# Optimization experiments

Measured on AMD Instinct MI355X. Metric: run time of the kernel, lower is better.

The kernel has to match this reference:

```python
import jax, jax.numpy as jnp
import numpy as np

LN_EPS = 1e-5


def lstm_cell(x, h, c, Wih, Whh, b):
    # PyTorch gate order: i, f, g, o
    gates = x @ Wih.T + h @ Whh.T + b
    i, f, g, o = jnp.split(gates, 4, axis=-1)
    c = jax.nn.sigmoid(f) * c + jax.nn.sigmoid(i) * jnp.tanh(g)
    h = jax.nn.sigmoid(o) * jnp.tanh(c)
    return h, c


def run_lstm_layer(xs, Wih, Whh, b, reverse=False):
    # xs: (T, B, D) -> ys: (T, B, H); zero initial state, matching nn.LSTM default
    B = xs.shape[1]
    H = Whh.shape[1]
    init = (jnp.zeros((B, H), xs.dtype), jnp.zeros((B, H), xs.dtype))

    def step(carry, x):
        h, c = lstm_cell(x, carry[0], carry[1], Wih, Whh, b)
        return (h, c), h

    _, ys = jax.lax.scan(step, init, xs, reverse=reverse)
    return ys


def forward(x, enc0_Wih, enc0_Whh, enc0_b, enc1_Wih, enc1_Whh, enc1_b,
            fc_z_W, fc_z_b, ln_g, ln_b, fc_init_W, fc_init_b,
            dec0_Wih, dec0_Whh, dec0_b, dec1_Wih, dec1_Whh, dec1_b,
            fc_out_W, fc_out_b):
    B, T, In = x.shape
    H = dec0_Whh.shape[1]
    L = 2  # num_layers

    # ---------- Encoder: 2-layer bidirectional LSTM ----------
    xs = jnp.transpose(x, (1, 0, 2))  # (T, B, In)
    # layer 0 (index 0 = forward dir, 1 = backward dir)
    f0 = run_lstm_layer(xs, enc0_Wih[0], enc0_Whh[0], enc0_b[0], reverse=False)
    b0 = run_lstm_layer(xs, enc0_Wih[1], enc0_Whh[1], enc0_b[1], reverse=True)
    h0cat = jnp.concatenate([f0, b0], axis=-1)  # (T, B, 2H); inter-layer dropout = identity (eval)
    # layer 1
    f1 = run_lstm_layer(h0cat, enc1_Wih[0], enc1_Whh[0], enc1_b[0], reverse=False)
    b1 = run_lstm_layer(h0cat, enc1_Wih[1], enc1_Whh[1], enc1_b[1], reverse=True)
    last_out = jnp.concatenate([f1[-1], b1[-1]], axis=-1)  # (B, 2H) == out[:, -1, :]

    zz = last_out @ fc_z_W.T + fc_z_b  # dropout = identity in eval
    mu = jnp.mean(zz, axis=-1, keepdims=True)
    var = jnp.mean((zz - mu) ** 2, axis=-1, keepdims=True)
    z = (zz - mu) * jax.lax.rsqrt(var + LN_EPS) * ln_g + ln_b  # (B, latent)

    # torch: fc_init(z).view(num_layers, batch, hidden) -- raw row-major reshape
    h_init = (z @ fc_init_W.T + fc_init_b).reshape(L, B, H)
    c_init = jnp.zeros_like(h_init)

    inp0 = jnp.zeros((B, In), x.dtype)

    def dec_step(carry, _):
        inp, h0, c0, h1, c1 = carry
        h0, c0 = lstm_cell(inp, h0, c0, dec0_Wih, dec0_Whh, dec0_b)
        h1, c1 = lstm_cell(h0, h1, c1, dec1_Wih, dec1_Whh, dec1_b)
        pred = h1 @ fc_out_W.T + fc_out_b  # dropout = identity (eval)
        # teacher_forcing_ratio = 0.0 path: feed back detached prediction
        return (jax.lax.stop_gradient(pred), h0, c0, h1, c1), pred

    carry0 = (inp0, h_init[0], c_init[0], h_init[1], c_init[1])
    _, preds = jax.lax.scan(dec_step, carry0, None, length=T)  # (T, B, In)
    x_hat = jnp.transpose(preds, (1, 0, 2))  # (B, T, In)
    return x_hat, z


def setup_inputs() -> dict:
    key = jax.random.key(0)
    B, T, In, H, Lat = 2048, 100, 64, 128, 32
    ks = iter(jax.random.split(key, 32))
    s = 0.08  # weight scale for stability
    d = {
        'x': jax.random.normal(next(ks), (B, T, In), jnp.float32),
        'enc0_Wih': s * jax.random.normal(next(ks), (2, 4 * H, In), jnp.float32),
        'enc0_Whh': s * jax.random.normal(next(ks), (2, 4 * H, H), jnp.float32),
        'enc0_b': s * jax.random.normal(next(ks), (2, 4 * H), jnp.float32),
        'enc1_Wih': s * jax.random.normal(next(ks), (2, 4 * H, 2 * H), jnp.float32),
        'enc1_Whh': s * jax.random.normal(next(ks), (2, 4 * H, H), jnp.float32),
        'enc1_b': s * jax.random.normal(next(ks), (2, 4 * H), jnp.float32),
        'fc_z_W': s * jax.random.normal(next(ks), (Lat, 2 * H), jnp.float32),
        'fc_z_b': s * jax.random.normal(next(ks), (Lat,), jnp.float32),
        'ln_g': jnp.ones((Lat,), jnp.float32),
        'ln_b': jnp.zeros((Lat,), jnp.float32),
        'fc_init_W': s * jax.random.normal(next(ks), (2 * H, Lat), jnp.float32),
        'fc_init_b': s * jax.random.normal(next(ks), (2 * H,), jnp.float32),
        'dec0_Wih': s * jax.random.normal(next(ks), (4 * H, In), jnp.float32),
        'dec0_Whh': s * jax.random.normal(next(ks), (4 * H, H), jnp.float32),
        'dec0_b': s * jax.random.normal(next(ks), (4 * H,), jnp.float32),
        'dec1_Wih': s * jax.random.normal(next(ks), (4 * H, H), jnp.float32),
        'dec1_Whh': s * jax.random.normal(next(ks), (4 * H, H), jnp.float32),
        'dec1_b': s * jax.random.normal(next(ks), (4 * H,), jnp.float32),
        'fc_out_W': s * jax.random.normal(next(ks), (In, H), jnp.float32),
        'fc_out_b': s * jax.random.normal(next(ks), (In,), jnp.float32),
    }
    return d


def reference(x, enc0_Wih, enc0_Whh, enc0_b, enc1_Wih, enc1_Whh, enc1_b,
              fc_z_W, fc_z_b, ln_g, ln_b, fc_init_W, fc_init_b,
              dec0_Wih, dec0_Whh, dec0_b, dec1_Wih, dec1_Whh, dec1_b,
              fc_out_W, fc_out_b):
    return forward(x, enc0_Wih, enc0_Whh, enc0_b, enc1_Wih, enc1_Whh, enc1_b,
                   fc_z_W, fc_z_b, ln_g, ln_b, fc_init_W, fc_init_b,
                   dec0_Wih, dec0_Whh, dec0_b, dec1_Wih, dec1_Whh, dec1_b,
                   fc_out_W, fc_out_b)
```

## Files before the change

### kernel.cpp

```cpp
#include <hip/hip_runtime.h>

using u32 = unsigned int;
using u16 = unsigned short;

typedef __attribute__((ext_vector_type(8))) short bfrag;
typedef __attribute__((ext_vector_type(4))) float f32x4;

constexpr int T_ = 100, B_ = 2048;
constexpr size_t X_HAT_SZ = (size_t)B_ * T_ * 64;

constexpr size_t PKB    = 26214400;
constexpr size_t PK_A0  = PKB + 0;
constexpr size_t PK_A1  = PKB + 32768;
constexpr size_t PK_A2  = PKB + 65536;
constexpr size_t PK_A3  = PKB + 131072;
constexpr size_t PK_A4  = PKB + 196608;
constexpr size_t PK_A5  = PKB + 327680;
constexpr size_t PK_A6  = PKB + 458752;
constexpr size_t PK_A7  = PKB + 524288;
constexpr size_t PK_A8  = PKB + 557056;
constexpr size_t PK_A9  = PKB + 622592;
constexpr size_t PK_A10 = PKB + 688128;
constexpr size_t PK_A11 = PKB + 753664;
constexpr size_t PK_ENDU = PKB + 761856;
constexpr size_t O_FCZT  = PK_ENDU * 2;
constexpr size_t O_FCIT  = O_FCZT + 32768;
constexpr size_t O_FINIT = O_FCIT + 32768;

__device__ __forceinline__ u16 f2bfu(float f) {
  u32 u = __float_as_uint(f);
  u += 0x7fffu + ((u >> 16) & 1u);
  return (u16)(u >> 16);
}
__device__ __forceinline__ float bf2f(u32 s) { return __uint_as_float(s << 16); }

__device__ __forceinline__ float sigf(float v) {
  return __builtin_amdgcn_rcpf(1.f + __expf(-v));
}
__device__ __forceinline__ float tanhfast(float v) {
  float a = fabsf(v);
  float e = __expf(-2.f * a);
  float t = fmaf(-2.f * e, __builtin_amdgcn_rcpf(1.f + e), 1.f);
  return v < 0.f ? -t : t;
}

__device__ __forceinline__ bfrag ldA(const u16* buf, int strideHalf, int kt, int lane) {
  return *(const bfrag*)(buf + (lane & 15) * strideHalf + kt * 32 + (lane >> 4) * 8);
}

template <int NKT>
__device__ __forceinline__ void mm(f32x4 acc[4], const bfrag* A, const u16* WP, int w, int lane) {
#pragma unroll
  for (int kt = 0; kt < NKT; ++kt) {
#pragma unroll
    for (int g = 0; g < 4; ++g) {
      bfrag bw = *(const bfrag*)(WP + (((size_t)(kt * 32 + g * 8 + w)) * 64 + lane) * 8);
      acc[g] = __builtin_amdgcn_mfma_f32_16x16x32_bf16(A[kt], bw, acc[g], 0, 0, 0);
    }
  }
}

template <int NKT>
__device__ __forceinline__ void loadW(bfrag* W, const u16* wsu, size_t base, int w, int lane) {
#pragma unroll
  for (int kt = 0; kt < NKT; ++kt)
#pragma unroll
    for (int g = 0; g < 4; ++g)
      W[kt * 4 + g] = *(const bfrag*)(wsu + base + (((size_t)(kt * 32 + g * 8 + w)) * 64 + lane) * 8);
}

template <int NKT>
__device__ __forceinline__ void mmR(f32x4 acc[4], const u16* lds, int sh, const bfrag* W, int lane) {
#pragma unroll
  for (int kt = 0; kt < NKT; ++kt) {
    bfrag a = ldA(lds, sh, kt, lane);
#pragma unroll
    for (int g = 0; g < 4; ++g)
      acc[g] = __builtin_amdgcn_mfma_f32_16x16x32_bf16(a, W[kt * 4 + g], acc[g], 0, 0, 0);
  }
}

template <int NKT>
__device__ __forceinline__ void mmL(f32x4 acc[4], const u16* alds, int sh,
                                    const u16* wlds, int w, int lane) {
#pragma unroll
  for (int kt = 0; kt < NKT; ++kt) {
    bfrag a = ldA(alds, sh, kt, lane);
#pragma unroll
    for (int g = 0; g < 4; ++g) {
      bfrag b = *(const bfrag*)(wlds + ((size_t)(kt * 32 + g * 8 + w) * 64 + lane) * 8);
      acc[g] = __builtin_amdgcn_mfma_f32_16x16x32_bf16(a, b, acc[g], 0, 0, 0);
    }
  }
}

__device__ __forceinline__ void cellfin(const f32x4 acc[4], float c[4], u16 hq[4]) {
#pragma unroll
  for (int q = 0; q < 4; ++q) {
    float iv = sigf(acc[0][q]);
    float fv = sigf(acc[1][q]);
    float gv = tanhfast(acc[2][q]);
    float ov = sigf(acc[3][q]);
    c[q] = fmaf(fv, c[q], iv * gv);
    hq[q] = f2bfu(ov * tanhfast(c[q]));
  }
}

__global__ void pack_kernel(const float* e0wih, const float* e0whh,
                            const float* e1wih, const float* e1whh,
                            const float* d0wih, const float* d0whh,
                            const float* d1wih, const float* d1whh,
                            const float* fczw, const float* fciw, const float* fcow,
                            char* ws) {
  int idx = blockIdx.x * 256 + threadIdx.x;
  u16* wsu = (u16*)ws;

  const float* srcs[12] = { e0wih, e0wih + 512 * 64, e0whh, e0whh + 512 * 128,
                            e1wih, e1wih + 512 * 256, e1whh,
                            d0wih, d0whh, d1wih, d1whh, fcow };
  const int Ks[12]  = { 64, 64, 128, 128, 256, 256, 128, 64, 128, 128, 128, 128 };
  const int NFs[12] = { 32, 32, 32, 32, 32, 32, 32, 32, 32, 32, 32, 4 };
  const int cnt[12] = { 32768, 32768, 65536, 65536, 131072, 131072, 65536,
                        32768, 65536, 65536, 65536, 8192 };
  const size_t dst[12] = { PK_A0, PK_A1, PK_A2, PK_A3, PK_A4, PK_A5, PK_A6,
                           PK_A7, PK_A8, PK_A9, PK_A10, PK_A11 };
#pragma unroll
  for (int p = 0; p < 12; ++p) {
    if (idx < cnt[p]) {
      int NF = NFs[p], K = Ks[p];
      int kt = idx / (NF * 512);
      int rem = idx - kt * NF * 512;
      int nf = rem >> 9;
      int li = rem & 511;
      int lane = li >> 3, j = li & 7;
      int n = nf * 16 + (lane & 15);
      int k = kt * 32 + (lane >> 4) * 8 + j;
      wsu[dst[p] + idx] = f2bfu(srcs[p][(size_t)n * K + k]);
      return;
    }
    idx -= cnt[p];
  }
  if (idx < 8192) {
    int k = idx >> 5, l = idx & 31;
    ((float*)(ws + O_FCZT))[idx] = fczw[(size_t)l * 256 + k];
    return;
  }
  idx -= 8192;
  if (idx < 8192) {
    int l = idx >> 8, o = idx & 255;
    ((float*)(ws + O_FCIT))[idx] = fciw[(size_t)o * 32 + l];
    return;
  }
}
constexpr int PACK_TOTAL = 761856 + 16384;
constexpr int PACK_GRID = (PACK_TOTAL + 255) / 256;

__global__ __launch_bounds__(512, 2) void enc01_kernel(
    const float* __restrict__ x, const float* __restrict__ e0b,
    char* __restrict__ ws, float* __restrict__ out) {
  __shared__ __align__(16) u16 xb[16 * 72];
  __shared__ __align__(16) u16 hA[16 * 136];

  const int tid = threadIdx.x;
  const int lane = tid & 63, w = tid >> 6;
  const int mode = blockIdx.x >> 7;
  const int chunk = blockIdx.x & 127;
  const int b0r = chunk * 16;
  const u16* wsu = (const u16*)ws;
  const int uu = 16 * w + (lane & 15);
  const int rg = lane >> 4;
  const bool rev = (mode == 0);
  u16* dst = rev ? (u16*)out : (u16*)ws;

  bfrag Wi[8], Wh[16];
  loadW<2>(Wi, wsu, rev ? PK_A1 : PK_A0, w, lane);
  loadW<4>(Wh, wsu, rev ? PK_A3 : PK_A2, w, lane);
  const float* bias = e0b + (rev ? 512 : 0);
  const float bi = bias[uu], bf = bias[128 + uu], bg = bias[256 + uu], bo = bias[384 + uu];

  const int xr = tid >> 5, xcp = (tid & 31) * 2;
  auto ldx = [&](int t) {
    return *(const float2*)(x + ((size_t)(b0r + xr) * T_ + t) * 64 + xcp);
  };

  for (int i = tid; i < 16 * 136; i += 512) hA[i] = 0;
  float c[4] = {0.f, 0.f, 0.f, 0.f};
  float2 pf = ldx(rev ? T_ - 1 : 0);
  *(u32*)&xb[xr * 72 + xcp] = ((u32)f2bfu(pf.y) << 16) | f2bfu(pf.x);
  __syncthreads();
  pf = ldx(rev ? T_ - 2 : 1);

  for (int s = 0; s < T_; ++s) {
    int t = rev ? T_ - 1 - s : s;
    f32x4 acc[4] = { {bi,bi,bi,bi}, {bf,bf,bf,bf}, {bg,bg,bg,bg}, {bo,bo,bo,bo} };
    mmR<2>(acc, xb, 72, Wi, lane);
    mmR<4>(acc, hA, 136, Wh, lane);
    u16 hq[4];
    cellfin(acc, c, hq);
    __syncthreads();
#pragma unroll
    for (int q = 0; q < 4; ++q) {
      int row = rg * 4 + q;
      hA[row * 136 + uu] = hq[q];
      dst[(((size_t)chunk * T_ + t) * 16 + row) * 128 + uu] = hq[q];
    }
    if (s < T_ - 1)
      *(u32*)&xb[xr * 72 + xcp] = ((u32)f2bfu(pf.y) << 16) | f2bfu(pf.x);
    if (s < T_ - 2) pf = ldx(rev ? t - 2 : t + 2);
    __syncthreads();
  }
}

constexpr int E2_A6   = 0;
constexpr int E2_CAT  = 131072;
constexpr int E2_HB   = 139520;
constexpr int E2_LAST = 0;
constexpr int E2_ZB   = 16384;

__global__ __launch_bounds__(512, 1) void enc2_kernel(
    const float* __restrict__ e1b, const float* __restrict__ fczb,
    const float* __restrict__ lng, const float* __restrict__ lnb,
    const float* __restrict__ fcib,
    char* __restrict__ ws, float* __restrict__ out) {
  __shared__ __align__(16) char sm[143872];
  u16* A6L = (u16*)(sm + E2_A6);
  u16* cat = (u16*)(sm + E2_CAT);
  u16* hB  = (u16*)(sm + E2_HB);

  const int tid = threadIdx.x;
  const int lane = tid & 63, w = tid >> 6;
  const int chunk = blockIdx.x;
  const int b0r = chunk * 16;
  const u16* wsu = (const u16*)ws;
  const int uu = 16 * w + (lane & 15);
  const int rg = lane >> 4;

  {
    const uint4* src = (const uint4*)(wsu + PK_A6);
    uint4* d = (uint4*)A6L;
    for (int i = tid; i < 8192; i += 512) d[i] = src[i];
  }
  bfrag W4[32];
  loadW<8>(W4, wsu, PK_A4, w, lane);
  const float bi = e1b[uu], bf = e1b[128 + uu], bg = e1b[256 + uu], bo = e1b[384 + uu];
  for (int i = tid; i < 16 * 136; i += 512) hB[i] = 0;
  float c[4] = {0.f, 0.f, 0.f, 0.f};

  const u32* f0u = (const u32*)ws;
  const u32* b0u = (const u32*)out;
  const int prow = tid >> 6, pc4 = tid & 63;
  auto ldrow = [&](const u32* src, int t, int r) {
    return src[(((size_t)chunk * T_ + t) * 16 + r) * 64 + pc4];
  };
  u32 pa = ldrow(f0u, 0, prow), pb = ldrow(f0u, 0, prow + 8);
  u32 pc = ldrow(b0u, 0, prow), pd = ldrow(b0u, 0, prow + 8);
  *(u32*)&cat[prow * 264 + pc4 * 2] = pa;
  *(u32*)&cat[(prow + 8) * 264 + pc4 * 2] = pb;
  *(u32*)&cat[prow * 264 + 128 + pc4 * 2] = pc;
  *(u32*)&cat[(prow + 8) * 264 + 128 + pc4 * 2] = pd;
  __syncthreads();
  pa = ldrow(f0u, 1, prow); pb = ldrow(f0u, 1, prow + 8);
  pc = ldrow(b0u, 1, prow); pd = ldrow(b0u, 1, prow + 8);

  for (int t = 0; t < T_; ++t) {
    f32x4 acc[4] = { {bi,bi,bi,bi}, {bf,bf,bf,bf}, {bg,bg,bg,bg}, {bo,bo,bo,bo} };
    mmR<8>(acc, cat, 264, W4, lane);
    mmL<4>(acc, hB, 136, A6L, w, lane);
    u16 hq[4];
    cellfin(acc, c, hq);
    __syncthreads();
#pragma unroll
    for (int q = 0; q < 4; ++q) hB[(rg * 4 + q) * 136 + uu] = hq[q];
    if (t < T_ - 1) {
      *(u32*)&cat[prow * 264 + pc4 * 2] = pa;
      *(u32*)&cat[(prow + 8) * 264 + pc4 * 2] = pb;
      *(u32*)&cat[prow * 264 + 128 + pc4 * 2] = pc;
      *(u32*)&cat[(prow + 8) * 264 + 128 + pc4 * 2] = pd;
    }
    if (t < T_ - 2) {
      pa = ldrow(f0u, t + 2, prow); pb = ldrow(f0u, t + 2, prow + 8);
      pc = ldrow(b0u, t + 2, prow); pd = ldrow(b0u, t + 2, prow + 8);
    }
    __syncthreads();
  }

  float* lastout = (float*)(sm + E2_LAST);
  float* zbuf = (float*)(sm + E2_ZB);
  {
    const float* b = e1b + 512;
    float bi2 = b[uu], bf2 = b[128 + uu], bg2 = b[256 + uu], bo2 = b[384 + uu];
    bfrag a8[8];
#pragma unroll
    for (int kt = 0; kt < 8; ++kt) a8[kt] = ldA(cat, 264, kt, lane);
    f32x4 acc[4] = { {bi2,bi2,bi2,bi2}, {bf2,bf2,bf2,bf2}, {bg2,bg2,bg2,bg2}, {bo2,bo2,bo2,bo2} };
    mm<8>(acc, a8, wsu + PK_A5, w, lane);
#pragma unroll
    for (int q = 0; q < 4; ++q) {
      float iv = sigf(acc[0][q]);
      float gv = tanhfast(acc[2][q]);
      float ov = sigf(acc[3][q]);
      float cv = iv * gv;
      lastout[(rg * 4 + q) * 256 + 128 + uu] = ov * tanhfast(cv);
    }
    for (int i = tid; i < 2048; i += 512) {
      int r = i >> 7, cc = i & 127;
      lastout[r * 256 + cc] = bf2f(hB[r * 136 + cc]);
    }
    __syncthreads();
  }

  {
    int r = tid >> 5, l = tid & 31;
    const float* fczT = (const float*)(ws + O_FCZT);
    float acc = fczb[l];
    for (int k = 0; k < 256; ++k) acc = fmaf(lastout[r * 256 + k], fczT[k * 32 + l], acc);
    float s1 = acc, s2 = acc * acc;
#pragma unroll
    for (int off = 16; off >= 1; off >>= 1) {
      s1 += __shfl_xor(s1, off, 32);
      s2 += __shfl_xor(s2, off, 32);
    }
    float mu = s1 * (1.f / 32.f);
    float var = s2 * (1.f / 32.f) - mu * mu;
    float zv = (acc - mu) * rsqrtf(var + 1e-5f) * lng[l] + lnb[l];
    zbuf[r * 32 + l] = zv;
    out[X_HAT_SZ + (size_t)(b0r + r) * 32 + l] = zv;
  }
  __syncthreads();

  {
    const float* fciT = (const float*)(ws + O_FCIT);
    float* finit = (float*)(ws + O_FINIT);
    int o = tid & 255, half = tid >> 8;
#pragma unroll
    for (int rr = 0; rr < 8; ++rr) {
      int r = half * 8 + rr;
      float acc = fcib[o];
#pragma unroll
      for (int l = 0; l < 32; ++l) acc = fmaf(zbuf[r * 32 + l], fciT[l * 256 + o], acc);
      finit[(size_t)(b0r + r) * 256 + o] = acc;
    }
  }
}

constexpr int DC_A10 = 0;
constexpr int DC_A11 = 131072;
constexpr int DC_XB  = 147456;
constexpr int DC_HA  = 149760;
constexpr int DC_HB  = 154112;
__global__ __launch_bounds__(512, 1) void dec_kernel(
    const float* __restrict__ d0b, const float* __restrict__ d1b,
    const float* __restrict__ fcob,
    char* __restrict__ ws, float* __restrict__ out) {
  __shared__ __align__(16) char sm[158464];
  u16* A10L = (u16*)(sm + DC_A10);
  u16* A11L = (u16*)(sm + DC_A11);
  u16* xb   = (u16*)(sm + DC_XB);
  u16* hA   = (u16*)(sm + DC_HA);
  u16* hB   = (u16*)(sm + DC_HB);

  const int tid = threadIdx.x;
  const int lane = tid & 63, w = tid >> 6;
  const int chunk = blockIdx.x;
  const int b0r = chunk * 16;
  const u16* wsu = (const u16*)ws;
  const float* finit = (const float*)(ws + O_FINIT);
  const int uu = 16 * w + (lane & 15);
  const int rg = lane >> 4;

  {
    const uint4* src = (const uint4*)(wsu + PK_A10);
    uint4* d = (uint4*)A10L;
    for (int i = tid; i < 9216; i += 512) d[i] = src[i];
  }
  bfrag W7[8], W8[16], W9[16];
  loadW<2>(W7, wsu, PK_A7, w, lane);
  loadW<4>(W8, wsu, PK_A8, w, lane);
  loadW<4>(W9, wsu, PK_A9, w, lane);

  for (int i = tid; i < 16 * 72; i += 512) xb[i] = 0;
  for (int i = tid; i < 2048; i += 512) {
    int r = i >> 7, j = i & 127;
    int b = b0r + r;
    hA[r * 136 + j] = f2bfu(finit[(size_t)(b >> 1) * 256 + (b & 1) * 128 + j]);
    hB[r * 136 + j] = f2bfu(finit[(size_t)(1024 + (b >> 1)) * 256 + (b & 1) * 128 + j]);
  }
  const float d0i = d0b[uu], d0f = d0b[128 + uu], d0g = d0b[256 + uu], d0o = d0b[384 + uu];
  const float d1i = d1b[uu], d1f = d1b[128 + uu], d1g = d1b[256 + uu], d1o = d1b[384 + uu];
  const float fob = (w < 4) ? fcob[16 * w + (lane & 15)] : 0.f;
  float c0[4] = {0.f, 0.f, 0.f, 0.f}, c1[4] = {0.f, 0.f, 0.f, 0.f};
  __syncthreads();

  for (int t = 0; t < T_; ++t) {
    f32x4 acc[4] = { {d0i,d0i,d0i,d0i}, {d0f,d0f,d0f,d0f}, {d0g,d0g,d0g,d0g}, {d0o,d0o,d0o,d0o} };
    mmR<2>(acc, xb, 72, W7, lane);
    mmR<4>(acc, hA, 136, W8, lane);
    u16 hq[4];
    cellfin(acc, c0, hq);
    __syncthreads();
#pragma unroll
    for (int q = 0; q < 4; ++q) hA[(rg * 4 + q) * 136 + uu] = hq[q];
    __syncthreads();
    f32x4 acc1[4] = { {d1i,d1i,d1i,d1i}, {d1f,d1f,d1f,d1f}, {d1g,d1g,d1g,d1g}, {d1o,d1o,d1o,d1o} };
    mmR<4>(acc1, hA, 136, W9, lane);
    mmL<4>(acc1, hB, 136, A10L, w, lane);
    u16 hq1[4];
    cellfin(acc1, c1, hq1);
    __syncthreads();
#pragma unroll
    for (int q = 0; q < 4; ++q) hB[(rg * 4 + q) * 136 + uu] = hq1[q];
    __syncthreads();
    if (w < 4) {
      f32x4 accP = {fob, fob, fob, fob};
#pragma unroll
      for (int kt = 0; kt < 4; ++kt) {
        bfrag a = ldA(hB, 136, kt, lane);
        bfrag b = *(const bfrag*)(A11L + ((size_t)(kt * 4 + w) * 64 + lane) * 8);
        accP = __builtin_amdgcn_mfma_f32_16x16x32_bf16(a, b, accP, 0, 0, 0);
      }
      int oc = 16 * w + (lane & 15);
#pragma unroll
      for (int q = 0; q < 4; ++q) {
        int row = rg * 4 + q;
        float p = accP[q];
        out[((size_t)(b0r + row) * T_ + t) * 64 + oc] = p;
        xb[row * 72 + oc] = f2bfu(p);
      }
    }
    __syncthreads();
  }
}

extern "C" void kernel_launch(void* const* d_in, const int* in_sizes, int n_in,
                              void* d_out, int out_size, void* d_ws, size_t ws_size,
                              hipStream_t stream) {
  const float* x     = (const float*)d_in[0];
  const float* e0wih = (const float*)d_in[1];
  const float* e0whh = (const float*)d_in[2];
  const float* e0b   = (const float*)d_in[3];
  const float* e1wih = (const float*)d_in[4];
  const float* e1whh = (const float*)d_in[5];
  const float* e1b   = (const float*)d_in[6];
  const float* fczw  = (const float*)d_in[7];
  const float* fczb  = (const float*)d_in[8];
  const float* lng   = (const float*)d_in[9];
  const float* lnb   = (const float*)d_in[10];
  const float* fciw  = (const float*)d_in[11];
  const float* fcib  = (const float*)d_in[12];
  const float* d0wih = (const float*)d_in[13];
  const float* d0whh = (const float*)d_in[14];
  const float* d0b   = (const float*)d_in[15];
  const float* d1wih = (const float*)d_in[16];
  const float* d1whh = (const float*)d_in[17];
  const float* d1b   = (const float*)d_in[18];
  const float* fcow  = (const float*)d_in[19];
  const float* fcob  = (const float*)d_in[20];
  char* ws = (char*)d_ws;
  float* out = (float*)d_out;

  pack_kernel<<<PACK_GRID, 256, 0, stream>>>(e0wih, e0whh, e1wih, e1whh,
                                             d0wih, d0whh, d1wih, d1whh,
                                             fczw, fciw, fcow, ws);
  enc01_kernel<<<256, 512, 0, stream>>>(x, e0b, ws, out);
  enc2_kernel<<<128, 512, 0, stream>>>(e1b, fczb, lng, lnb, fcib, ws, out);
  dec_kernel<<<128, 512, 0, stream>>>(d0b, d1b, fcob, ws, out);
}
```

Before: 585.8 us.

## Double-buffer LDS state to halve barriers and pin weights in AGPRs

The hidden-state and input staging buffers in the encoder and decoder kernels become ping-pong LDS buffers. Each step can then write the next state without first waiting on a barrier, which removes one __syncthreads per recurrent stage. Weight fragments are pinned into accumulator registers with empty inline asm, and the decoder's fc_out weights move from LDS into registers. Launch attributes now request two waves per EU, which may force register spills or prevent two blocks from fitting given the large LDS allocations.

```diff
diff --git a/kernel.cpp b/kernel.cpp
--- a/kernel.cpp
+++ b/kernel.cpp
@@ -44,6 +44,12 @@
   return v < 0.f ? -t : t;
 }
 
+template <int N>
+__device__ __forceinline__ void pinA(bfrag* W) {
+#pragma unroll
+  for (int i = 0; i < N; ++i) asm volatile("" : "+a"(W[i]));
+}
+
 __device__ __forceinline__ bfrag ldA(const u16* buf, int strideHalf, int kt, int lane) {
   return *(const bfrag*)(buf + (lane & 15) * strideHalf + kt * 32 + (lane >> 4) * 8);
 }
@@ -155,11 +161,12 @@
 constexpr int PACK_TOTAL = 761856 + 16384;
 constexpr int PACK_GRID = (PACK_TOTAL + 255) / 256;
 
-__global__ __launch_bounds__(512, 2) void enc01_kernel(
+__global__ __attribute__((amdgpu_flat_work_group_size(512, 512), amdgpu_waves_per_eu(2, 2)))
+void enc01_kernel(
     const float* __restrict__ x, const float* __restrict__ e0b,
     char* __restrict__ ws, float* __restrict__ out) {
-  __shared__ __align__(16) u16 xb[16 * 72];
-  __shared__ __align__(16) u16 hA[16 * 136];
+  __shared__ __align__(16) u16 xbuf[2][16 * 72];
+  __shared__ __align__(16) u16 hbuf[2][16 * 136];
 
   const int tid = threadIdx.x;
   const int lane = tid & 63, w = tid >> 6;
@@ -175,6 +182,8 @@
   bfrag Wi[8], Wh[16];
   loadW<2>(Wi, wsu, rev ? PK_A1 : PK_A0, w, lane);
   loadW<4>(Wh, wsu, rev ? PK_A3 : PK_A2, w, lane);
+  pinA<8>(Wi);
+  pinA<16>(Wh);
   const float* bias = e0b + (rev ? 512 : 0);
   const float bi = bias[uu], bf = bias[128 + uu], bg = bias[256 + uu], bo = bias[384 + uu];
 
@@ -183,49 +192,49 @@
     return *(const float2*)(x + ((size_t)(b0r + xr) * T_ + t) * 64 + xcp);
   };
 
-  for (int i = tid; i < 16 * 136; i += 512) hA[i] = 0;
+  for (int i = tid; i < 2 * 16 * 136; i += 512) (&hbuf[0][0])[i] = 0;
   float c[4] = {0.f, 0.f, 0.f, 0.f};
   float2 pf = ldx(rev ? T_ - 1 : 0);
-  *(u32*)&xb[xr * 72 + xcp] = ((u32)f2bfu(pf.y) << 16) | f2bfu(pf.x);
+  *(u32*)&xbuf[0][xr * 72 + xcp] = ((u32)f2bfu(pf.y) << 16) | f2bfu(pf.x);
   __syncthreads();
   pf = ldx(rev ? T_ - 2 : 1);
 
+  int p = 0;
   for (int s = 0; s < T_; ++s) {
     int t = rev ? T_ - 1 - s : s;
     f32x4 acc[4] = { {bi,bi,bi,bi}, {bf,bf,bf,bf}, {bg,bg,bg,bg}, {bo,bo,bo,bo} };
-    mmR<2>(acc, xb, 72, Wi, lane);
-    mmR<4>(acc, hA, 136, Wh, lane);
+    mmR<2>(acc, xbuf[p], 72, Wi, lane);
+    mmR<4>(acc, hbuf[p], 136, Wh, lane);
     u16 hq[4];
     cellfin(acc, c, hq);
-    __syncthreads();
 #pragma unroll
     for (int q = 0; q < 4; ++q) {
       int row = rg * 4 + q;
-      hA[row * 136 + uu] = hq[q];
+      hbuf[1 - p][row * 136 + uu] = hq[q];
       dst[(((size_t)chunk * T_ + t) * 16 + row) * 128 + uu] = hq[q];
     }
     if (s < T_ - 1)
-      *(u32*)&xb[xr * 72 + xcp] = ((u32)f2bfu(pf.y) << 16) | f2bfu(pf.x);
+      *(u32*)&xbuf[1 - p][xr * 72 + xcp] = ((u32)f2bfu(pf.y) << 16) | f2bfu(pf.x);
     if (s < T_ - 2) pf = ldx(rev ? t - 2 : t + 2);
     __syncthreads();
+    p ^= 1;
   }
 }
 
 constexpr int E2_A6   = 0;
 constexpr int E2_CAT  = 131072;
-constexpr int E2_HB   = 139520;
+constexpr int E2_HB   = 147968;
 constexpr int E2_LAST = 0;
 constexpr int E2_ZB   = 16384;
 
-__global__ __launch_bounds__(512, 1) void enc2_kernel(
+__global__ __attribute__((amdgpu_flat_work_group_size(512, 512), amdgpu_waves_per_eu(2, 2)))
+void enc2_kernel(
     const float* __restrict__ e1b, const float* __restrict__ fczb,
     const float* __restrict__ lng, const float* __restrict__ lnb,
     const float* __restrict__ fcib,
     char* __restrict__ ws, float* __restrict__ out) {
-  __shared__ __align__(16) char sm[143872];
+  __shared__ __align__(16) char sm[156672];
   u16* A6L = (u16*)(sm + E2_A6);
-  u16* cat = (u16*)(sm + E2_CAT);
-  u16* hB  = (u16*)(sm + E2_HB);
 
   const int tid = threadIdx.x;
   const int lane = tid & 63, w = tid >> 6;
@@ -242,8 +251,12 @@
   }
   bfrag W4[32];
   loadW<8>(W4, wsu, PK_A4, w, lane);
+  pinA<32>(W4);
   const float bi = e1b[uu], bf = e1b[128 + uu], bg = e1b[256 + uu], bo = e1b[384 + uu];
-  for (int i = tid; i < 16 * 136; i += 512) hB[i] = 0;
+  {
+    u16* hb0 = (u16*)(sm + E2_HB);
+    for (int i = tid; i < 2 * 16 * 136; i += 512) hb0[i] = 0;
+  }
   float c[4] = {0.f, 0.f, 0.f, 0.f};
 
   const u32* f0u = (const u32*)ws;
@@ -254,46 +267,57 @@
   };
   u32 pa = ldrow(f0u, 0, prow), pb = ldrow(f0u, 0, prow + 8);
   u32 pc = ldrow(b0u, 0, prow), pd = ldrow(b0u, 0, prow + 8);
-  *(u32*)&cat[prow * 264 + pc4 * 2] = pa;
-  *(u32*)&cat[(prow + 8) * 264 + pc4 * 2] = pb;
-  *(u32*)&cat[prow * 264 + 128 + pc4 * 2] = pc;
-  *(u32*)&cat[(prow + 8) * 264 + 128 + pc4 * 2] = pd;
+  {
+    u16* cat0 = (u16*)(sm + E2_CAT);
+    *(u32*)&cat0[prow * 264 + pc4 * 2] = pa;
+    *(u32*)&cat0[(prow + 8) * 264 + pc4 * 2] = pb;
+    *(u32*)&cat0[prow * 264 + 128 + pc4 * 2] = pc;
+    *(u32*)&cat0[(prow + 8) * 264 + 128 + pc4 * 2] = pd;
+  }
   __syncthreads();
   pa = ldrow(f0u, 1, prow); pb = ldrow(f0u, 1, prow + 8);
   pc = ldrow(b0u, 1, prow); pd = ldrow(b0u, 1, prow + 8);
 
+  int p = 0;
   for (int t = 0; t < T_; ++t) {
+    u16* catP = (u16*)(sm + E2_CAT + p * 8448);
+    u16* catN = (u16*)(sm + E2_CAT + (1 - p) * 8448);
+    u16* hbP  = (u16*)(sm + E2_HB + p * 4352);
+    u16* hbN  = (u16*)(sm + E2_HB + (1 - p) * 4352);
     f32x4 acc[4] = { {bi,bi,bi,bi}, {bf,bf,bf,bf}, {bg,bg,bg,bg}, {bo,bo,bo,bo} };
-    mmR<8>(acc, cat, 264, W4, lane);
-    mmL<4>(acc, hB, 136, A6L, w, lane);
-    u16 hq[4];
-    cellfin(acc, c, hq);
-    __syncthreads();
-#pragma unroll
-    for (int q = 0; q < 4; ++q) hB[(rg * 4 + q) * 136 + uu] = hq[q];
+    mmR<8>(acc, catP, 264, W4, lane);
+    mmL<4>(acc, hbP, 136, A6L, w, lane);
     if (t < T_ - 1) {
-      *(u32*)&cat[prow * 264 + pc4 * 2] = pa;
-      *(u32*)&cat[(prow + 8) * 264 + pc4 * 2] = pb;
-      *(u32*)&cat[prow * 264 + 128 + pc4 * 2] = pc;
-      *(u32*)&cat[(prow + 8) * 264 + 128 + pc4 * 2] = pd;
+      *(u32*)&catN[prow * 264 + pc4 * 2] = pa;
+      *(u32*)&catN[(prow + 8) * 264 + pc4 * 2] = pb;
+      *(u32*)&catN[prow * 264 + 128 + pc4 * 2] = pc;
+      *(u32*)&catN[(prow + 8) * 264 + 128 + pc4 * 2] = pd;
     }
     if (t < T_ - 2) {
       pa = ldrow(f0u, t + 2, prow); pb = ldrow(f0u, t + 2, prow + 8);
       pc = ldrow(b0u, t + 2, prow); pd = ldrow(b0u, t + 2, prow + 8);
     }
-    __syncthreads();
+    u16 hq[4];
+    cellfin(acc, c, hq);
+#pragma unroll
+    for (int q = 0; q < 4; ++q) hbN[(rg * 4 + q) * 136 + uu] = hq[q];
+    __syncthreads();
+    p ^= 1;
   }
 
   float* lastout = (float*)(sm + E2_LAST);
   float* zbuf = (float*)(sm + E2_ZB);
   {
+    u16* cat99 = (u16*)(sm + E2_CAT + 8448);
+    u16* hb99  = (u16*)(sm + E2_HB);
     const float* b = e1b + 512;
     float bi2 = b[uu], bf2 = b[128 + uu], bg2 = b[256 + uu], bo2 = b[384 + uu];
     bfrag a8[8];
 #pragma unroll
-    for (int kt = 0; kt < 8; ++kt) a8[kt] = ldA(cat, 264, kt, lane);
+    for (int kt = 0; kt < 8; ++kt) a8[kt] = ldA(cat99, 264, kt, lane);
     f32x4 acc[4] = { {bi2,bi2,bi2,bi2}, {bf2,bf2,bf2,bf2}, {bg2,bg2,bg2,bg2}, {bo2,bo2,bo2,bo2} };
     mm<8>(acc, a8, wsu + PK_A5, w, lane);
+    __syncthreads();
 #pragma unroll
     for (int q = 0; q < 4; ++q) {
       float iv = sigf(acc[0][q]);
@@ -304,7 +328,7 @@
     }
     for (int i = tid; i < 2048; i += 512) {
       int r = i >> 7, cc = i & 127;
-      lastout[r * 256 + cc] = bf2f(hB[r * 136 + cc]);
+      lastout[r * 256 + cc] = bf2f(hb99[r * 136 + cc]);
     }
     __syncthreads();
   }
@@ -344,20 +368,16 @@
 }
 
 constexpr int DC_A10 = 0;
-constexpr int DC_A11 = 131072;
-constexpr int DC_XB  = 147456;
-constexpr int DC_HA  = 149760;
-constexpr int DC_HB  = 154112;
-__global__ __launch_bounds__(512, 1) void dec_kernel(
+constexpr int DC_XB  = 131072;
+constexpr int DC_HA  = 135680;
+constexpr int DC_HB  = 144384;
+__global__ __attribute__((amdgpu_flat_work_group_size(512, 512), amdgpu_waves_per_eu(2, 2)))
+void dec_kernel(
     const float* __restrict__ d0b, const float* __restrict__ d1b,
     const float* __restrict__ fcob,
     char* __restrict__ ws, float* __restrict__ out) {
-  __shared__ __align__(16) char sm[158464];
+  __shared__ __align__(16) char sm[153088];
   u16* A10L = (u16*)(sm + DC_A10);
-  u16* A11L = (u16*)(sm + DC_A11);
-  u16* xb   = (u16*)(sm + DC_XB);
-  u16* hA   = (u16*)(sm + DC_HA);
-  u16* hB   = (u16*)(sm + DC_HB);
 
   const int tid = threadIdx.x;
   const int lane = tid & 63, w = tid >> 6;
@@ -371,19 +391,34 @@
   {
     const uint4* src = (const uint4*)(wsu + PK_A10);
     uint4* d = (uint4*)A10L;
-    for (int i = tid; i < 9216; i += 512) d[i] = src[i];
-  }
-  bfrag W7[8], W8[16], W9[16];
+    for (int i = tid; i < 8192; i += 512) d[i] = src[i];
+  }
+  bfrag W7[8], W8[16], W9[16], W11[4];
   loadW<2>(W7, wsu, PK_A7, w, lane);
   loadW<4>(W8, wsu, PK_A8, w, lane);
   loadW<4>(W9, wsu, PK_A9, w, lane);
-
-  for (int i = tid; i < 16 * 72; i += 512) xb[i] = 0;
-  for (int i = tid; i < 2048; i += 512) {
-    int r = i >> 7, j = i & 127;
-    int b = b0r + r;
-    hA[r * 136 + j] = f2bfu(finit[(size_t)(b >> 1) * 256 + (b & 1) * 128 + j]);
-    hB[r * 136 + j] = f2bfu(finit[(size_t)(1024 + (b >> 1)) * 256 + (b & 1) * 128 + j]);
+  {
+    int wf = w & 3;
+#pragma unroll
+    for (int kt = 0; kt < 4; ++kt)
+      W11[kt] = *(const bfrag*)(wsu + PK_A11 + (((size_t)(kt * 4 + wf)) * 64 + lane) * 8);
+  }
+  pinA<8>(W7);
+  pinA<16>(W8);
+  pinA<16>(W9);
+  pinA<4>(W11);
+
+  {
+    u16* xb0 = (u16*)(sm + DC_XB);
+    for (int i = tid; i < 2 * 16 * 72; i += 512) xb0[i] = 0;
+    u16* ha0 = (u16*)(sm + DC_HA);
+    u16* hb0 = (u16*)(sm + DC_HB);
+    for (int i = tid; i < 2048; i += 512) {
+      int r = i >> 7, j = i & 127;
+      int b = b0r + r;
+      ha0[r * 136 + j] = f2bfu(finit[(size_t)(b >> 1) * 256 + (b & 1) * 128 + j]);
+      hb0[r * 136 + j] = f2bfu(finit[(size_t)(1024 + (b >> 1)) * 256 + (b & 1) * 128 + j]);
+    }
   }
   const float d0i = d0b[uu], d0f = d0b[128 + uu], d0g = d0b[256 + uu], d0o = d0b[384 + uu];
   const float d1i = d1b[uu], d1f = d1b[128 + uu], d1g = d1b[256 + uu], d1o = d1b[384 + uu];
@@ -391,43 +426,52 @@
   float c0[4] = {0.f, 0.f, 0.f, 0.f}, c1[4] = {0.f, 0.f, 0.f, 0.f};
   __syncthreads();
 
+  int p = 0;
   for (int t = 0; t < T_; ++t) {
-    f32x4 acc[4] = { {d0i,d0i,d0i,d0i}, {d0f,d0f,d0f,d0f}, {d0g,d0g,d0g,d0g}, {d0o,d0o,d0o,d0o} };
-    mmR<2>(acc, xb, 72, W7, lane);
-    mmR<4>(acc, hA, 136, W8, lane);
-    u16 hq[4];
-    cellfin(acc, c0, hq);
-    __syncthreads();
-#pragma unroll
-    for (int q = 0; q < 4; ++q) hA[(rg * 4 + q) * 136 + uu] = hq[q];
-    __syncthreads();
-    f32x4 acc1[4] = { {d1i,d1i,d1i,d1i}, {d1f,d1f,d1f,d1f}, {d1g,d1g,d1g,d1g}, {d1o,d1o,d1o,d1o} };
-    mmR<4>(acc1, hA, 136, W9, lane);
-    mmL<4>(acc1, hB, 136, A10L, w, lane);
-    u16 hq1[4];
-    cellfin(acc1, c1, hq1);
-    __syncthreads();
-#pragma unroll
-    for (int q = 0; q < 4; ++q) hB[(rg * 4 + q) * 136 + uu] = hq1[q];
+    u16* xbP = (u16*)(sm + DC_XB + p * 2304);
+    u16* xbN = (u16*)(sm + DC_XB + (1 - p) * 2304);
+    u16* haP = (u16*)(sm + DC_HA + p * 4352);
+    u16* haN = (u16*)(sm + DC_HA + (1 - p) * 4352);
+    u16* hbP = (u16*)(sm + DC_HB + p * 4352);
+    u16* hbN = (u16*)(sm + DC_HB + (1 - p) * 4352);
+    {
+      f32x4 acc[4] = { {d0i,d0i,d0i,d0i}, {d0f,d0f,d0f,d0f}, {d0g,d0g,d0g,d0g}, {d0o,d0o,d0o,d0o} };
+      mmR<2>(acc, xbP, 72, W7, lane);
+      mmR<4>(acc, haP, 136, W8, lane);
+      u16 hq[4];
+      cellfin(acc, c0, hq);
+#pragma unroll
+      for (int q = 0; q < 4; ++q) haN[(rg * 4 + q) * 136 + uu] = hq[q];
+    }
+    __syncthreads();
+    {
+      f32x4 acc[4] = { {d1i,d1i,d1i,d1i}, {d1f,d1f,d1f,d1f}, {d1g,d1g,d1g,d1g}, {d1o,d1o,d1o,d1o} };
+      mmR<4>(acc, haN, 136, W9, lane);
+      mmL<4>(acc, hbP, 136, A10L, w, lane);
+      u16 hq[4];
+      cellfin(acc, c1, hq);
+#pragma unroll
+      for (int q = 0; q < 4; ++q) hbN[(rg * 4 + q) * 136 + uu] = hq[q];
+    }
     __syncthreads();
     if (w < 4) {
       f32x4 accP = {fob, fob, fob, fob};
 #pragma unroll
       for (int kt = 0; kt < 4; ++kt) {
-        bfrag a = ldA(hB, 136, kt, lane);
-        bfrag b = *(const bfrag*)(A11L + ((size_t)(kt * 4 + w) * 64 + lane) * 8);
-        accP = __builtin_amdgcn_mfma_f32_16x16x32_bf16(a, b, accP, 0, 0, 0);
+        bfrag a = ldA(hbN, 136, kt, lane);
+        accP = __builtin_amdgcn_mfma_f32_16x16x32_bf16(a, W11[kt], accP, 0, 0, 0);
       }
       int oc = 16 * w + (lane & 15);
 #pragma unroll
       for (int q = 0; q < 4; ++q) {
         int row = rg * 4 + q;
-        float p = accP[q];
-        out[((size_t)(b0r + row) * T_ + t) * 64 + oc] = p;
-        xb[row * 72 + oc] = f2bfu(p);
+        float pv = accP[q];
+        out[((size_t)(b0r + row) * T_ + t) * 64 + oc] = pv;
+        xbN[row * 72 + oc] = f2bfu(pv);
       }
     }
     __syncthreads();
+    p ^= 1;
   }
 }
 
```

After: 622.9 us. 6.3% more time.
